# Performance work log

Hardware: AMD Instinct MI355X
Metric: run time of the kernel (lower is better)

The kernel has to match this reference:

```python
import jax, jax.numpy as jnp
import numpy as np

N = 50000      # nodes
E = 1600000    # edges (avg degree 32)
D = 256        # in_dim
H = 256        # hid
L = 3          # num_layers (all layer input dims equal D==H)
EPS_LN = 1e-5  # torch LayerNorm default eps
EPS_DEN = 1e-8 # denom clamp from the module


def setup_inputs() -> dict:
    key = jax.random.key(0)
    ks = jax.random.split(key, 6)
    x = jax.random.normal(ks[0], (N, D), dtype=jnp.float32)
    edge_index = jax.random.randint(ks[1], (2, E), 0, N, dtype=jnp.int32)
    # stacked per-layer params (all layers share dims since in_dim == hid)
    W_sage = jax.random.normal(ks[2], (L, 2 * D, H), dtype=jnp.float32) * 0.02
    b_sage = jnp.zeros((L, H), dtype=jnp.float32)
    gamma = jnp.ones((L, H), dtype=jnp.float32)
    beta = jnp.zeros((L, H), dtype=jnp.float32)
    W_attn = jax.random.normal(ks[3], (L, 2 * D), dtype=jnp.float32) * 0.02
    b_attn = jnp.zeros((L,), dtype=jnp.float32)
    W_skip = jax.random.normal(ks[4], (D, H), dtype=jnp.float32) * 0.02
    b_skip = jnp.zeros((H,), dtype=jnp.float32)
    return {"x": x, "edge_index": edge_index, "W_sage": W_sage, "b_sage": b_sage,
            "gamma": gamma, "beta": beta, "W_attn": W_attn, "b_attn": b_attn,
            "W_skip": W_skip, "b_skip": b_skip}


def reference(x, edge_index, W_sage, b_sage, gamma, beta, W_attn, b_attn, W_skip, b_skip):
    src, dst = edge_index[0], edge_index[1]
    residual = x @ W_skip + b_skip  # (N, H)
    h = x
    for i in range(L):
        d = h.shape[1]
        # edge attention: attn_lin(cat([x[dst], x[src]])) == (x@w_dst)[dst] + (x@w_src)[src] + b
        w = W_attn[i]
        s_dst = h @ w[:d]          # (N,)
        s_src = h @ w[d:]          # (N,)
        raw = s_dst[dst] + s_src[src] + b_attn[i]   # (E,)
        a = jnp.exp(raw)
        denom = jax.ops.segment_sum(a, dst, num_segments=N)        # (N,)
        alpha = a / jnp.maximum(denom[dst], EPS_DEN)               # (E,)
        agg = jax.ops.segment_sum(alpha[:, None] * h[src], dst, num_segments=N)  # (N, d)
        # SAGE linear on cat([h, agg]) + LayerNorm + ReLU
        z = jnp.concatenate([h, agg], axis=-1) @ W_sage[i] + b_sage[i]  # (N, H)
        mu = z.mean(axis=-1, keepdims=True)
        var = z.var(axis=-1, keepdims=True)
        h = jax.nn.relu(gamma[i] * (z - mu) / jnp.sqrt(var + EPS_LN) + beta[i])
    return (h + residual).mean(axis=0)  # (H,)
```

## Files before the change

kernel.cpp:

```cpp
#include <hip/hip_runtime.h>
#include <hip/hip_bf16.h>

#define NN 50000
#define EE 1600000
#define DIM 256
#define KDIM 512
#define NLAYER 3
#define NRANGE 8
#define RNODES (NN / NRANGE)
#define CAP 80

using bf16x8 = __attribute__((ext_vector_type(8))) short;
using f32x4  = __attribute__((ext_vector_type(4))) float;
using f32x2  = __attribute__((ext_vector_type(2))) float;

static __device__ __forceinline__ unsigned short f2bf(float f) {
    unsigned u = __builtin_bit_cast(unsigned, f);
    unsigned r = (u + 0x7FFFu + ((u >> 16) & 1u)) >> 16;
    return (unsigned short)r;
}
static __device__ __forceinline__ float bf2f(unsigned short s) {
    return __builtin_bit_cast(float, (unsigned)s << 16);
}

static __device__ __forceinline__ void gload_lds16(const void* g, void* l) {
    __builtin_amdgcn_global_load_lds(
        reinterpret_cast<const __attribute__((address_space(1))) void*>(
            reinterpret_cast<uintptr_t>(g)),
        reinterpret_cast<__attribute__((address_space(3))) void*>(
            static_cast<unsigned>(reinterpret_cast<uintptr_t>(l))),
        16, 0, 0);
}

#if defined(__has_builtin) && __has_builtin(__builtin_amdgcn_cvt_pk_f32_fp8) && __has_builtin(__builtin_amdgcn_cvt_pk_fp8_f32)
#define FP8_NATIVE 1
#else
#define FP8_NATIVE 0
#endif

template <bool HI>
static __device__ __forceinline__ f32x2 fp8x2_dec(unsigned w) {
#if FP8_NATIVE
    return __builtin_amdgcn_cvt_pk_f32_fp8((int)w, HI);
#else
    unsigned v = HI ? (w >> 16) : w;
    unsigned b0 = v & 0xFFu, b1 = (v >> 8) & 0xFFu;
    unsigned u0 = ((b0 & 0x80u) << 24) | ((b0 & 0x7Fu) << 20);
    unsigned u1 = ((b1 & 0x80u) << 24) | ((b1 & 0x7Fu) << 20);
    f32x2 r;
    r[0] = __builtin_bit_cast(float, u0) * 0x1p120f;
    r[1] = __builtin_bit_cast(float, u1) * 0x1p120f;
    return r;
#endif
}

#if !FP8_NATIVE
static __device__ __forceinline__ unsigned fp8_enc1(float f) {
    unsigned u = __builtin_bit_cast(unsigned, f * 0x1p-120f);
    unsigned s = (u >> 24) & 0x80u;
    unsigned m = u & 0x7FFFFFFFu;
    m = m + 0x7FFFFu + ((m >> 20) & 1u);
    return s | ((m >> 20) & 0x7Fu);
}
#endif

static __device__ __forceinline__ unsigned fp8x4_enc(float a, float b, float c, float d) {
#if FP8_NATIVE
    int w = __builtin_amdgcn_cvt_pk_fp8_f32(a, b, 0, false);
    w = __builtin_amdgcn_cvt_pk_fp8_f32(c, d, w, true);
    return (unsigned)w;
#else
    return fp8_enc1(a) | (fp8_enc1(b) << 8) | (fp8_enc1(c) << 16) | (fp8_enc1(d) << 24);
#endif
}

static __device__ __forceinline__ void fp8x8_fma(float* acc, uint2 r, float wg) {
    f32x2 p0 = fp8x2_dec<false>(r.x);
    f32x2 p1 = fp8x2_dec<true>(r.x);
    f32x2 p2 = fp8x2_dec<false>(r.y);
    f32x2 p3 = fp8x2_dec<true>(r.y);
    acc[0] += wg * p0[0]; acc[1] += wg * p0[1];
    acc[2] += wg * p1[0]; acc[3] += wg * p1[1];
    acc[4] += wg * p2[0]; acc[5] += wg * p2[1];
    acc[6] += wg * p3[0]; acc[7] += wg * p3[1];
}

__global__ __launch_bounds__(256) void k_prep(const float* __restrict__ x,
                                              const float* __restrict__ w_src,
                                              unsigned short* __restrict__ hout,
                                              unsigned char* __restrict__ f8out,
                                              float* __restrict__ e_src) {
    int wave = threadIdx.x >> 6, lane = threadIdx.x & 63;
    int n = blockIdx.x * 4 + wave;
    if (n >= NN) return;
    const float4 v = *reinterpret_cast<const float4*>(x + (size_t)n * DIM + lane * 4);
    const float4 wv = *reinterpret_cast<const float4*>(w_src + lane * 4);
    float sc = v.x * wv.x + v.y * wv.y + v.z * wv.z + v.w * wv.w;
    #pragma unroll
    for (int m = 32; m; m >>= 1) sc += __shfl_xor(sc, m);
    if (lane == 0) e_src[n] = __expf(sc);
    ushort4 o;
    o.x = f2bf(v.x); o.y = f2bf(v.y); o.z = f2bf(v.z); o.w = f2bf(v.w);
    *reinterpret_cast<ushort4*>(hout + (size_t)n * DIM + lane * 4) = o;
    *reinterpret_cast<unsigned*>(f8out + (size_t)n * DIM + lane * 4) =
        fp8x4_enc(v.x, v.y, v.z, v.w);
}

__global__ __launch_bounds__(256) void k_scatter(const int* __restrict__ ei, int* __restrict__ cursor,
                                                 unsigned short* __restrict__ csr) {
    const int range = blockIdx.x & (NRANGE - 1);
    const int lo = range * RNODES, hi = lo + RNODES;
    const int stride = (gridDim.x >> 3) * 256;
    for (int e = (blockIdx.x >> 3) * 256 + threadIdx.x; e < EE; e += stride) {
        int d = ei[EE + e];
        if (d >= lo && d < hi) {
            int pos = atomicAdd(&cursor[d], 1);
            if (pos < CAP) csr[d * CAP + pos] = (unsigned short)ei[e];
        }
    }
}

__global__ __launch_bounds__(256) void k_aggregate(const unsigned char* __restrict__ f8,
                                                   const float* __restrict__ e_src,
                                                   const int* __restrict__ cursor,
                                                   const unsigned short* __restrict__ csr,
                                                   unsigned short* __restrict__ agg) {
    int wave = threadIdx.x >> 6, lane = threadIdx.x & 63;
    int n = blockIdx.x * 4 + wave;
    if (n >= NN) return;
    int deg = cursor[n];
    if (deg > CAP) deg = CAP;
    const unsigned short* row = csr + (size_t)n * CAP;
    const int half = lane >> 5;
    const int col8 = (lane & 31) * 8;

    float acc[8] = {0.f, 0.f, 0.f, 0.f, 0.f, 0.f, 0.f, 0.f};
    float den = 0.f;

    int p = 0;
    #pragma unroll 2
    for (; p + 8 <= deg; p += 8) {
        int b = p + 4 * half;
        int s0 = row[b + 0];
        int s1 = row[b + 1];
        int s2 = row[b + 2];
        int s3 = row[b + 3];
        float w0 = e_src[s0], w1 = e_src[s1], w2 = e_src[s2], w3 = e_src[s3];
        uint2 r0 = *reinterpret_cast<const uint2*>(f8 + (size_t)s0 * DIM + col8);
        uint2 r1 = *reinterpret_cast<const uint2*>(f8 + (size_t)s1 * DIM + col8);
        uint2 r2 = *reinterpret_cast<const uint2*>(f8 + (size_t)s2 * DIM + col8);
        uint2 r3 = *reinterpret_cast<const uint2*>(f8 + (size_t)s3 * DIM + col8);
        fp8x8_fma(acc, r0, w0);
        fp8x8_fma(acc, r1, w1);
        fp8x8_fma(acc, r2, w2);
        fp8x8_fma(acc, r3, w3);
        den += (w0 + w1) + (w2 + w3);
    }
    for (; p < deg; p += 2) {
        int idx = p + half;
        bool valid = idx < deg;
        int s0 = row[valid ? idx : 0];
        float w0 = valid ? e_src[s0] : 0.f;
        uint2 r0 = *reinterpret_cast<const uint2*>(f8 + (size_t)s0 * DIM + col8);
        fp8x8_fma(acc, r0, w0);
        den += w0;
    }

    den += __shfl_xor(den, 32);
    float inv = (deg > 0) ? 1.f / den : 0.f;
    #pragma unroll
    for (int j = 0; j < 8; ++j) acc[j] += __shfl_xor(acc[j], 32);

    if (half == 0) {
        bf16x8 o;
        #pragma unroll
        for (int j = 0; j < 8; ++j) o[j] = (short)f2bf(acc[j] * inv);
        *reinterpret_cast<bf16x8*>(agg + (size_t)n * DIM + col8) = o;
    }
}

__global__ __launch_bounds__(256) void k_packB(const float* __restrict__ W, unsigned short* __restrict__ Bp) {
    int tid = blockIdx.x * 256 + threadIdx.x;
    int j    = tid & 7;
    int lane = (tid >> 3) & 63;
    int nf   = (tid >> 9) & 15;
    int ks   = tid >> 13;
    int c = lane & 15, q = lane >> 4;
    Bp[tid] = f2bf(W[(size_t)(ks * 32 + q * 8 + j) * DIM + nf * 16 + c]);
}

#define LDS_STRIDE 264
__global__ __launch_bounds__(256) void k_gemm_ln(const unsigned short* __restrict__ hin,
                                                 const unsigned short* __restrict__ agg,
                                                 const unsigned short* __restrict__ Bp,
                                                 const float* __restrict__ bias,
                                                 const float* __restrict__ gamma_l,
                                                 const float* __restrict__ beta_l,
                                                 const float* __restrict__ w_src_next,
                                                 unsigned short* __restrict__ hout,
                                                 unsigned char* __restrict__ f8out,
                                                 float* __restrict__ e_src) {
    __shared__ __align__(16) unsigned char lds_raw[4 * 16 * LDS_STRIDE * 2];
    unsigned short* bbuf0 = (unsigned short*)lds_raw;
    unsigned short* bbuf1 = bbuf0 + 8192;
    int w = threadIdx.x >> 6, lane = threadIdx.x & 63;
    int c = lane & 15, q = lane >> 4;
    int m0 = blockIdx.x * 64 + w * 16;

    auto stage = [&](int ks, unsigned short* buf) {
        const unsigned short* g = Bp + (size_t)ks * 8192 + w * 2048 + lane * 8;
        unsigned short* l = buf + w * 2048;
        #pragma unroll
        for (int i = 0; i < 4; ++i)
            gload_lds16(g + i * 512, l + i * 512);
    };

    f32x4 acc[16];
    #pragma unroll
    for (int nf = 0; nf < 16; ++nf) {
        float b = bias[nf * 16 + c];
        acc[nf] = (f32x4){b, b, b, b};
    }

    stage(0, bbuf0);
    bf16x8 a_cur = *reinterpret_cast<const bf16x8*>(hin + (size_t)(m0 + c) * DIM + q * 8);
    __syncthreads();

    #pragma unroll
    for (int ks = 0; ks < 16; ++ks) {
        const unsigned short* bb = (ks & 1) ? bbuf1 : bbuf0;
        unsigned short* bnext    = (ks & 1) ? bbuf0 : bbuf1;
        bf16x8 a_next = a_cur;
        if (ks + 1 < 16) {
            stage(ks + 1, bnext);
            const int kk1 = (ks + 1) * 32;
            const unsigned short* hs = (kk1 < DIM) ? hin : agg;
            a_next = *reinterpret_cast<const bf16x8*>(
                hs + (size_t)(m0 + c) * DIM + (kk1 & (DIM - 1)) + q * 8);
        }
        #pragma unroll
        for (int nf = 0; nf < 16; ++nf) {
            bf16x8 bfr = *reinterpret_cast<const bf16x8*>(bb + nf * 512 + lane * 8);
            acc[nf] = __builtin_amdgcn_mfma_f32_16x16x32_bf16(a_cur, bfr, acc[nf], 0, 0, 0);
        }
        __syncthreads();
        a_cur = a_next;
    }

    #pragma unroll
    for (int r = 0; r < 4; ++r) {
        float s = 0.f, s2 = 0.f;
        #pragma unroll
        for (int nf = 0; nf < 16; ++nf) {
            float v = acc[nf][r];
            s += v; s2 += v * v;
        }
        #pragma unroll
        for (int msk = 1; msk < 16; msk <<= 1) {
            s  += __shfl_xor(s, msk);
            s2 += __shfl_xor(s2, msk);
        }
        float mu = s * (1.f / DIM);
        float var = s2 * (1.f / DIM) - mu * mu;
        float rstd = rsqrtf(var + 1e-5f);
        float sc = 0.f;
        #pragma unroll
        for (int nf = 0; nf < 16; ++nf) {
            float v = fmaxf(gamma_l[nf * 16 + c] * (acc[nf][r] - mu) * rstd + beta_l[nf * 16 + c], 0.f);
            acc[nf][r] = v;
            if (w_src_next) sc += v * w_src_next[nf * 16 + c];
        }
        if (w_src_next) {
            #pragma unroll
            for (int msk = 1; msk < 16; msk <<= 1) sc += __shfl_xor(sc, msk);
            int row = m0 + q * 4 + r;
            if (c == 0 && row < NN) e_src[row] = __expf(sc);
        }
    }

    unsigned short* myl = (unsigned short*)lds_raw + w * 16 * LDS_STRIDE;
    #pragma unroll
    for (int nf = 0; nf < 16; ++nf) {
        #pragma unroll
        for (int r = 0; r < 4; ++r)
            myl[(q * 4 + r) * LDS_STRIDE + nf * 16 + c] = f2bf(acc[nf][r]);
    }
    #pragma unroll
    for (int i = 0; i < 8; ++i) {
        int row16 = 2 * i + (lane >> 5);
        bf16x8 v = *reinterpret_cast<const bf16x8*>(myl + row16 * LDS_STRIDE + (lane & 31) * 8);
        int grow = m0 + row16;
        if (grow < NN) {
            *reinterpret_cast<bf16x8*>(hout + (size_t)grow * DIM + (lane & 31) * 8) = v;
            if (f8out) {
                uint2 pk;
                pk.x = fp8x4_enc(bf2f((unsigned short)v[0]), bf2f((unsigned short)v[1]),
                                 bf2f((unsigned short)v[2]), bf2f((unsigned short)v[3]));
                pk.y = fp8x4_enc(bf2f((unsigned short)v[4]), bf2f((unsigned short)v[5]),
                                 bf2f((unsigned short)v[6]), bf2f((unsigned short)v[7]));
                *reinterpret_cast<uint2*>(f8out + (size_t)grow * DIM + (lane & 31) * 8) = pk;
            }
        }
    }
}

__global__ __launch_bounds__(256) void k_colsum_f32(const float* __restrict__ mat, float* __restrict__ out) {
    int j = threadIdx.x;
    float s = 0.f;
    for (int r = blockIdx.x; r < NN; r += gridDim.x) s += mat[(size_t)r * DIM + j];
    atomicAdd(&out[j], s);
}
__global__ __launch_bounds__(256) void k_colsum_bf16(const unsigned short* __restrict__ mat,
                                                     float* __restrict__ out) {
    int j = threadIdx.x;
    float s = 0.f;
    for (int r = blockIdx.x; r < NN; r += gridDim.x) s += bf2f(mat[(size_t)r * DIM + j]);
    atomicAdd(&out[j], s);
}

__global__ __launch_bounds__(256) void k_final(const float* __restrict__ hsum, const float* __restrict__ xsum,
                                               const float* __restrict__ W_skip, const float* __restrict__ b_skip,
                                               float* __restrict__ out) {
    int j = threadIdx.x;
    float acc = 0.f;
    const float invN = 1.f / (float)NN;
    for (int i = 0; i < DIM; ++i) acc += (xsum[i] * invN) * W_skip[(size_t)i * DIM + j];
    out[j] = hsum[j] * invN + acc + b_skip[j];
}

extern "C" void kernel_launch(void* const* d_in, const int* in_sizes, int n_in,
                              void* d_out, int out_size, void* d_ws, size_t ws_size,
                              hipStream_t stream) {
    const float* x      = (const float*)d_in[0];
    const int*   ei     = (const int*)d_in[1];
    const float* W_sage = (const float*)d_in[2];
    const float* b_sage = (const float*)d_in[3];
    const float* gamma  = (const float*)d_in[4];
    const float* beta   = (const float*)d_in[5];
    const float* W_attn = (const float*)d_in[6];
    const float* W_skip = (const float*)d_in[8];
    const float* b_skip = (const float*)d_in[9];
    float* out = (float*)d_out;

    const size_t ND = (size_t)NN * DIM;
    unsigned short* hx   = (unsigned short*)d_ws;
    unsigned short* hA   = hx + ND;
    unsigned short* hB   = hA + ND;
    unsigned short* agg  = hB + ND;
    unsigned short* Bp   = agg + ND;
    unsigned char*  f8a  = (unsigned char*)(Bp + (size_t)KDIM * DIM + 64);
    unsigned char*  f8b  = f8a + ND;
    float* e_src  = (float*)(f8b + ND + 64);
    float* colsum = e_src + NN;
    float* xsum   = colsum + DIM;
    int*   cursor = (int*)(xsum + DIM);
    unsigned short* csr = (unsigned short*)(cursor + NN);

    const int NBLK_RANGED = NRANGE * 784;

    hipError_t err;
    err = hipMemsetAsync(cursor, 0, (size_t)NN * sizeof(int), stream); (void)err;
    err = hipMemsetAsync(colsum, 0, 2 * DIM * sizeof(float), stream); (void)err;

    k_scatter<<<NBLK_RANGED, 256, 0, stream>>>(ei, cursor, csr);

    k_prep<<<NN / 4, 256, 0, stream>>>(x, W_attn + DIM, hx, f8a, e_src);

    unsigned short* hbufs[3] = {hx, hA, hB};
    unsigned char*  f8bufs[3] = {f8a, f8b, f8a};
    for (int l = 0; l < NLAYER; ++l) {
        unsigned short* h_in  = hbufs[l];
        unsigned short* h_out = hbufs[l + 1 < 3 ? l + 1 : 1];
        k_packB<<<(KDIM * DIM) / 256, 256, 0, stream>>>(W_sage + (size_t)l * KDIM * DIM, Bp);
        k_aggregate<<<NN / 4, 256, 0, stream>>>(f8bufs[l], e_src, cursor, csr, agg);
        const float* wnext = (l < NLAYER - 1) ? (W_attn + (size_t)(l + 1) * KDIM + DIM) : nullptr;
        unsigned char* f8next = (l < NLAYER - 1) ? f8bufs[l + 1] : nullptr;
        k_gemm_ln<<<(NN + 63) / 64, 256, 0, stream>>>(
            h_in, agg, Bp, b_sage + (size_t)l * DIM,
            gamma + (size_t)l * DIM, beta + (size_t)l * DIM,
            wnext, h_out, f8next, e_src);
    }

    k_colsum_bf16<<<256, 256, 0, stream>>>(hbufs[1], colsum);
    k_colsum_f32<<<256, 256, 0, stream>>>(x, xsum);
    k_final<<<1, 256, 0, stream>>>(colsum, xsum, W_skip, b_skip, out);
}
```

Measured before the change: 529.6 us.

## Pre-bucket edges by destination range before CSR scatter

Replaces the range-filtered scatter, where each of the 8 destination ranges rescanned the full edge list, with a two-pass bucketing step. One pass counts edges per range and the next writes packed (local dst, src) words into per-range buckets. The scatter then reads only its own range's bucket. This removes the eightfold re-reading of the edge list at the cost of two extra launches, a bucket buffer write and read, and a fixed BCAP capacity that could drop edges if a range overflows.

```diff
diff --git a/kernel.cpp b/kernel.cpp
--- a/kernel.cpp
+++ b/kernel.cpp
@@ -9,6 +9,9 @@
 #define NRANGE 8
 #define RNODES (NN / NRANGE)
 #define CAP 80
+#define TILE_E 4096
+#define NB_E ((EE + TILE_E - 1) / TILE_E)
+#define BCAP 210000
 
 using bf16x8 = __attribute__((ext_vector_type(8))) short;
 using f32x4  = __attribute__((ext_vector_type(4))) float;
@@ -106,17 +109,55 @@
         fp8x4_enc(v.x, v.y, v.z, v.w);
 }
 
-__global__ __launch_bounds__(256) void k_scatter(const int* __restrict__ ei, int* __restrict__ cursor,
+__global__ __launch_bounds__(256) void k_bkt_count(const int* __restrict__ ei,
+                                                   int* __restrict__ bcount,
+                                                   int* __restrict__ bbase) {
+    __shared__ int cnt[NRANGE];
+    int t = threadIdx.x;
+    if (t < NRANGE) cnt[t] = 0;
+    __syncthreads();
+    int e0 = blockIdx.x * TILE_E;
+    int e1 = min(e0 + TILE_E, EE);
+    for (int e = e0 + t; e < e1; e += 256)
+        atomicAdd(&cnt[ei[EE + e] / RNODES], 1);
+    __syncthreads();
+    if (t < NRANGE) bbase[blockIdx.x * NRANGE + t] = atomicAdd(&bcount[t], cnt[t]);
+}
+
+__global__ __launch_bounds__(256) void k_bkt_fill(const int* __restrict__ ei,
+                                                  const int* __restrict__ bbase,
+                                                  unsigned* __restrict__ bucket) {
+    __shared__ int pos[NRANGE];
+    __shared__ int bas[NRANGE];
+    int t = threadIdx.x;
+    if (t < NRANGE) { pos[t] = 0; bas[t] = bbase[blockIdx.x * NRANGE + t]; }
+    __syncthreads();
+    int e0 = blockIdx.x * TILE_E;
+    int e1 = min(e0 + TILE_E, EE);
+    for (int e = e0 + t; e < e1; e += 256) {
+        int d = ei[EE + e];
+        int s = ei[e];
+        int r = d / RNODES;
+        int p = atomicAdd(&pos[r], 1);
+        int idx = bas[r] + p;
+        if (idx < BCAP)
+            bucket[(size_t)r * BCAP + idx] = ((unsigned)(d - r * RNODES) << 16) | (unsigned)s;
+    }
+}
+
+__global__ __launch_bounds__(256) void k_scatter(const unsigned* __restrict__ bucket,
+                                                 const int* __restrict__ bcount,
+                                                 int* __restrict__ cursor,
                                                  unsigned short* __restrict__ csr) {
-    const int range = blockIdx.x & (NRANGE - 1);
-    const int lo = range * RNODES, hi = lo + RNODES;
+    const int r = blockIdx.x & (NRANGE - 1);
+    const int cnt = min(bcount[r], BCAP);
+    const int lo = r * RNODES;
     const int stride = (gridDim.x >> 3) * 256;
-    for (int e = (blockIdx.x >> 3) * 256 + threadIdx.x; e < EE; e += stride) {
-        int d = ei[EE + e];
-        if (d >= lo && d < hi) {
-            int pos = atomicAdd(&cursor[d], 1);
-            if (pos < CAP) csr[d * CAP + pos] = (unsigned short)ei[e];
-        }
+    for (int i = (blockIdx.x >> 3) * 256 + threadIdx.x; i < cnt; i += stride) {
+        unsigned e = bucket[(size_t)r * BCAP + i];
+        int d = lo + (int)(e >> 16);
+        int p = atomicAdd(&cursor[d], 1);
+        if (p < CAP) csr[(size_t)d * CAP + p] = (unsigned short)(e & 0xFFFFu);
     }
 }
 
@@ -354,15 +395,18 @@
     float* colsum = e_src + NN;
     float* xsum   = colsum + DIM;
     int*   cursor = (int*)(xsum + DIM);
-    unsigned short* csr = (unsigned short*)(cursor + NN);
-
-    const int NBLK_RANGED = NRANGE * 784;
+    int*   bcount = cursor + NN;
+    int*   bbase  = bcount + NRANGE;
+    unsigned short* csr = (unsigned short*)(bbase + NB_E * NRANGE);
+    unsigned* bucket = (unsigned*)(csr + (size_t)NN * CAP);
 
     hipError_t err;
-    err = hipMemsetAsync(cursor, 0, (size_t)NN * sizeof(int), stream); (void)err;
+    err = hipMemsetAsync(cursor, 0, (size_t)(NN + NRANGE) * sizeof(int), stream); (void)err;
     err = hipMemsetAsync(colsum, 0, 2 * DIM * sizeof(float), stream); (void)err;
 
-    k_scatter<<<NBLK_RANGED, 256, 0, stream>>>(ei, cursor, csr);
+    k_bkt_count<<<NB_E, 256, 0, stream>>>(ei, bcount, bbase);
+    k_bkt_fill<<<NB_E, 256, 0, stream>>>(ei, bbase, bucket);
+    k_scatter<<<NRANGE * 98, 256, 0, stream>>>(bucket, bcount, cursor, csr);
 
     k_prep<<<NN / 4, 256, 0, stream>>>(x, W_attn + DIM, hx, f8a, e_src);
 
```

Result: slower. 546.4 us (+3.2%).
